# Performance work log

Hardware: AMD Instinct MI355X
Metric: run time of the kernel (lower is better)

## Reference

```python
import jax, jax.numpy as jnp
import numpy as np

HEADS = 8
EPS = 1e-5
CONV_DIMS = [(16, 32), (32, 64), (64, 128), (128, 256), (256, 128), (128, 128)]


def _bn(x, g, b):
    # BatchNorm over the node dimension (training-mode batch statistics)
    m = x.mean(0)
    v = x.var(0)
    return (x - m) * jax.lax.rsqrt(v + EPS) * g + b


def _feast(x, src, dst, W, U, c, bias, n):
    # FeaStConv: q_h = softmax_h(u_h.(x_j - x_i) + c_h); out_i = mean_j sum_h q_h * (W_h x_j) + bias
    q = jax.nn.softmax((x[src] - x[dst]) @ U + c, axis=-1)          # [E, H]
    f = (x[src] @ W).reshape(src.shape[0], HEADS, -1)               # [E, H, C_out]
    msg = jnp.einsum('ehc,eh->ec', f, q)                            # [E, C_out]
    agg = jax.ops.segment_sum(msg, dst, num_segments=n)
    cnt = jax.ops.segment_sum(jnp.ones_like(dst, dtype=msg.dtype), dst, num_segments=n)
    return agg / cnt[:, None] + bias


def reference(pos, x, g0, b0, lin0_W, lin0_b,
              W0, U0, C0, B0, gc0, bc0,
              W1, U1, C1, B1, gc1, bc1,
              W2, U2, C2, B2, gc2, bc2,
              W3, U3, C3, B3, gc3, bc3,
              W4, U4, C4, B4, gc4, bc4,
              W5, U5, C5, B5, gc5, bc5,
              lin1_W, lin1_b, lin2_W, lin2_b, edge_index):
    n = pos.shape[0]
    loops = jnp.arange(n, dtype=edge_index.dtype)                   # PyG FeaStConv adds self-loops
    src = jnp.concatenate([edge_index[0], loops])
    dst = jnp.concatenate([edge_index[1], loops])

    h = _bn(pos, g0, b0)
    h = jnp.concatenate([h, x], axis=1)
    h = jax.nn.relu(h @ lin0_W + lin0_b)

    convs = [(W0, U0, C0, B0, gc0, bc0), (W1, U1, C1, B1, gc1, bc1),
             (W2, U2, C2, B2, gc2, bc2), (W3, U3, C3, B3, gc3, bc3),
             (W4, U4, C4, B4, gc4, bc4), (W5, U5, C5, B5, gc5, bc5)]
    for W, U, c, bias, g, b in convs:
        h = _feast(h, src, dst, W, U, c, bias, n)
        h = jax.nn.relu(_bn(h, g, b))

    h = jax.nn.relu(h @ lin1_W + lin1_b)
    return h @ lin2_W + lin2_b


def setup_inputs() -> dict:
    key = jax.random.key(0)
    N, E = 10000, 160000
    ks = iter(jax.random.split(key, 64))
    d = {}
    d['pos'] = jax.random.normal(next(ks), (N, 2), jnp.float32)
    d['x'] = jax.random.normal(next(ks), (N, 2), jnp.float32)
    d['edge_index'] = jax.random.randint(next(ks), (2, E), 0, N, dtype=jnp.int32)

    def lin(k, i, o):
        return jax.random.normal(k, (i, o), jnp.float32) * np.float32(1.0 / np.sqrt(i))

    d['g0'] = jnp.ones(2, jnp.float32); d['b0'] = jnp.zeros(2, jnp.float32)
    d['lin0_W'] = lin(next(ks), 4, 16); d['lin0_b'] = jnp.zeros(16, jnp.float32)
    for i, (ci, co) in enumerate(CONV_DIMS):
        d[f'W{i}'] = lin(next(ks), ci, HEADS * co)
        d[f'U{i}'] = lin(next(ks), ci, HEADS)
        d[f'C{i}'] = jnp.zeros(HEADS, jnp.float32)
        d[f'B{i}'] = jnp.zeros(co, jnp.float32)
        d[f'gc{i}'] = jnp.ones(co, jnp.float32)
        d[f'bc{i}'] = jnp.zeros(co, jnp.float32)
    d['lin1_W'] = lin(next(ks), 128, 64); d['lin1_b'] = jnp.zeros(64, jnp.float32)
    d['lin2_W'] = lin(next(ks), 64, 2); d['lin2_b'] = jnp.zeros(2, jnp.float32)
    return d
```

## Files before the change

kernel.cpp:

```cpp
#include <hip/hip_runtime.h>
#include <hip/hip_bf16.h>
#include <math.h>

#define HEADS 8
#define EPS 1e-5f

typedef __attribute__((ext_vector_type(8))) _Float16 half8;
typedef __attribute__((ext_vector_type(4))) _Float16 half4;
typedef __attribute__((ext_vector_type(2))) _Float16 half2v;
typedef __attribute__((ext_vector_type(4))) float f32x4;

__device__ __forceinline__ unsigned short f2h(float f) {
    union { _Float16 h; unsigned short u; } v;
    v.h = (_Float16)f;
    return v.u;
}

__global__ void k_deg(const int* __restrict__ ei, int* __restrict__ deg, int E, int N) {
    int e = blockIdx.x * blockDim.x + threadIdx.x;
    int E2 = E + N;
    if (e >= E2) return;
    int dst = (e < E) ? ei[E + e] : (e - E);
    atomicAdd(&deg[dst], 1);
}

__global__ void k_scan(const int* __restrict__ deg, int* __restrict__ row_ptr, int n) {
    __shared__ int part[1024];
    int t = threadIdx.x;
    int chunk = (n + 1023) >> 10;
    int begin = t * chunk;
    int end = begin + chunk;
    if (begin > n) begin = n;
    if (end > n) end = n;
    int s = 0;
    for (int i = begin; i < end; ++i) s += deg[i];
    part[t] = s;
    __syncthreads();
    for (int off = 1; off < 1024; off <<= 1) {
        int v = (t >= off) ? part[t - off] : 0;
        __syncthreads();
        part[t] += v;
        __syncthreads();
    }
    int run = (t == 0) ? 0 : part[t - 1];
    for (int i = begin; i < end; ++i) { row_ptr[i] = run; run += deg[i]; }
    if (t == 1023) row_ptr[n] = part[1023];
}

__global__ void k_fill(const int* __restrict__ ei, const int* __restrict__ row_ptr,
                       int* __restrict__ fill, int* __restrict__ src_sorted, int E, int N) {
    int e = blockIdx.x * blockDim.x + threadIdx.x;
    int E2 = E + N;
    if (e >= E2) return;
    int srcv, dst;
    if (e < E) { srcv = ei[e]; dst = ei[E + e]; } else { srcv = e - E; dst = srcv; }
    int p = atomicAdd(&fill[dst], 1);
    src_sorted[row_ptr[dst] + p] = srcv;
}

__global__ void k_pack(const float* __restrict__ W0, const float* __restrict__ W1,
                       const float* __restrict__ W2, const float* __restrict__ W3,
                       const float* __restrict__ W4, const float* __restrict__ W5,
                       unsigned short* __restrict__ Bp) {
    int idx = blockIdx.x * blockDim.x + threadIdx.x;
    const int CI[6]  = {16, 32, 64, 128, 256, 128};
    const int CO[6]  = {32, 64, 128, 256, 128, 128};
    const int COP[6] = {64, 64, 128, 256, 128, 128};
    const int OFF[7] = {0, 8192, 24576, 90112, 352256, 614400, 745472};
    if (idx >= OFF[6]) return;
    int L = 0;
    while (idx >= OFF[L + 1]) ++L;
    const float* W = L == 0 ? W0 : L == 1 ? W1 : L == 2 ? W2 : L == 3 ? W3 : L == 4 ? W4 : W5;
    int rel = idx - OFF[L];
    int j = rel & 7;
    int lane = (rel >> 3) & 63;
    int t = rel >> 9;
    int nT = COP[L] >> 4;
    int nt = t % nT, kt = t / nT;
    int kk = kt * 32 + ((lane >> 4) << 3) + j;
    int c  = (nt << 4) + (lane & 15);
    int ci = CI[L], co = CO[L];
    float v = 0.f;
    if (c < co) {
        int h = kk / ci, ko = kk % ci;
        v = W[ko * (HEADS * co) + h * co + c];
    }
    Bp[idx] = f2h(v);
}

__global__ void k_pos_stats(const float* __restrict__ pos, float* __restrict__ stats, int n) {
    int gid = blockIdx.x * blockDim.x + threadIdx.x;
    int stride = gridDim.x * blockDim.x;
    float s0 = 0, s1 = 0, q0 = 0, q1 = 0;
    for (int i = gid; i < n; i += stride) {
        float a = pos[i * 2], b = pos[i * 2 + 1];
        s0 += a; s1 += b; q0 += a * a; q1 += b * b;
    }
    __shared__ float red[256][4];
    int t = threadIdx.x;
    red[t][0] = s0; red[t][1] = s1; red[t][2] = q0; red[t][3] = q1;
    __syncthreads();
    for (int off = 128; off > 0; off >>= 1) {
        if (t < off) {
            red[t][0] += red[t + off][0]; red[t][1] += red[t + off][1];
            red[t][2] += red[t + off][2]; red[t][3] += red[t + off][3];
        }
        __syncthreads();
    }
    if (t == 0) {
        atomicAdd(&stats[0], red[0][0]); atomicAdd(&stats[1], red[0][1]);
        atomicAdd(&stats[2], red[0][2]); atomicAdd(&stats[3], red[0][3]);
    }
}

__global__ void k_front(const float* __restrict__ pos, const float* __restrict__ x,
                        const float* __restrict__ stats, const float* __restrict__ g0,
                        const float* __restrict__ b0, const float* __restrict__ W,
                        const float* __restrict__ bias, const float* __restrict__ U0,
                        _Float16* __restrict__ out, float* __restrict__ xu0, int n) {
    int i = blockIdx.x * blockDim.x + threadIdx.x;
    if (i >= n) return;
    float invn = 1.0f / (float)n;
    float in4[4];
    #pragma unroll
    for (int j = 0; j < 2; ++j) {
        float m = stats[j] * invn;
        float v = stats[2 + j] * invn - m * m;
        in4[j] = (pos[i * 2 + j] - m) * rsqrtf(v + EPS) * g0[j] + b0[j];
    }
    in4[2] = x[i * 2]; in4[3] = x[i * 2 + 1];
    float o16[16];
    #pragma unroll
    for (int o = 0; o < 16; ++o) {
        float s = bias[o];
        #pragma unroll
        for (int j = 0; j < 4; ++j) s += in4[j] * W[j * 16 + o];
        o16[o] = fmaxf(s, 0.f);
        out[i * 16 + o] = (_Float16)o16[o];
    }
    #pragma unroll
    for (int hh = 0; hh < 8; ++hh) {
        float p = 0.f;
        #pragma unroll
        for (int k = 0; k < 16; ++k) p += o16[k] * U0[k * 8 + hh];
        xu0[i * 8 + hh] = p;
    }
}

__device__ __forceinline__ void chunk_softmax(const float* __restrict__ xu,
        const int* __restrict__ srcs, int base, int cnt, int lane,
        float4 xi0, float4 xi1, float4 c0, float4 c1, float dinv,
        float* __restrict__ qrow , int* __restrict__ srow ) {
    if (lane < cnt) {
        int s = srcs[base + lane];
        float4 xs0 = *(const float4*)(xu + (size_t)s * 8);
        float4 xs1 = *(const float4*)(xu + (size_t)s * 8 + 4);
        float t[8];
        t[0] = xs0.x - xi0.x + c0.x; t[1] = xs0.y - xi0.y + c0.y;
        t[2] = xs0.z - xi0.z + c0.z; t[3] = xs0.w - xi0.w + c0.w;
        t[4] = xs1.x - xi1.x + c1.x; t[5] = xs1.y - xi1.y + c1.y;
        t[6] = xs1.z - xi1.z + c1.z; t[7] = xs1.w - xi1.w + c1.w;
        float mx = t[0];
        #pragma unroll
        for (int h = 1; h < 8; ++h) mx = fmaxf(mx, t[h]);
        float sum = 0.f;
        #pragma unroll
        for (int h = 0; h < 8; ++h) { t[h] = __expf(t[h] - mx); sum += t[h]; }
        float qs = dinv / sum;
        float4 q0 = {t[0] * qs, t[1] * qs, t[2] * qs, t[3] * qs};
        float4 q1 = {t[4] * qs, t[5] * qs, t[6] * qs, t[7] * qs};
        *(float4*)(qrow + lane * 8) = q0;
        *(float4*)(qrow + lane * 8 + 4) = q1;
        srow[lane] = s;
    }
}

template<int V>
__global__ __launch_bounds__(256) void k_gather_big(const _Float16* __restrict__ hin,
        const float* __restrict__ xu, const float* __restrict__ chead,
        const int* __restrict__ row_ptr, const int* __restrict__ srcs,
        unsigned short* __restrict__ S, int n, int ci) {
    __shared__ float qbuf[4][64 * 8];
    __shared__ int   sbuf[4][64];
    int w = threadIdx.x >> 6, lane = threadIdx.x & 63;
    int i = blockIdx.x * 4 + w;
    if (i >= n) return;
    int rp0 = row_ptr[i], rp1 = row_ptr[i + 1];
    float dinv = 1.f / (float)(rp1 - rp0);
    float4 xi0 = *(const float4*)(xu + (size_t)i * 8);
    float4 xi1 = *(const float4*)(xu + (size_t)i * 8 + 4);
    float4 c0 = *(const float4*)chead;
    float4 c1 = *(const float4*)(chead + 4);
    int kb = lane * V;
    float acc[8][V];
    #pragma unroll
    for (int hh = 0; hh < 8; ++hh)
        #pragma unroll
        for (int v = 0; v < V; ++v) acc[hh][v] = 0.f;

    for (int base = rp0; base < rp1; base += 64) {
        int cnt = rp1 - base; if (cnt > 64) cnt = 64;
        chunk_softmax(xu, srcs, base, cnt, lane, xi0, xi1, c0, c1, dinv, qbuf[w], sbuf[w]);
        for (int j = 0; j < cnt; ++j) {
            int s = sbuf[w][j];
            const float4* qr = (const float4*)(qbuf[w] + j * 8);
            float4 q0 = qr[0], q1 = qr[1];
            float q[8] = {q0.x, q0.y, q0.z, q0.w, q1.x, q1.y, q1.z, q1.w};
            const _Float16* hs = hin + (size_t)s * ci + kb;
            float xv[V];
            if (V == 4) { half4 f = *(const half4*)hs; xv[0] = (float)f[0]; xv[1] = (float)f[1]; xv[2] = (float)f[2]; xv[3] = (float)f[3]; }
            else if (V == 2) { half2v f = *(const half2v*)hs; xv[0] = (float)f[0]; xv[1] = (float)f[1]; }
            else xv[0] = (float)hs[0];
            #pragma unroll
            for (int hh = 0; hh < 8; ++hh)
                #pragma unroll
                for (int v = 0; v < V; ++v) acc[hh][v] += q[hh] * xv[v];
        }
    }
    #pragma unroll
    for (int hh = 0; hh < 8; ++hh) {
        unsigned short o[V];
        #pragma unroll
        for (int v = 0; v < V; ++v) o[v] = f2h(acc[hh][v]);
        unsigned short* sp = S + (size_t)i * 8 * ci + hh * ci + kb;
        if (V == 4)      *(ushort4*)sp = *(ushort4*)o;
        else if (V == 2) *(ushort2*)sp = *(ushort2*)o;
        else             sp[0] = o[0];
    }
}

template<int V2>
__global__ __launch_bounds__(256) void k_gather_small(const _Float16* __restrict__ hin,
        const float* __restrict__ xu, const float* __restrict__ chead,
        const int* __restrict__ row_ptr, const int* __restrict__ srcs,
        unsigned short* __restrict__ S, int n) {
    const int ci = 8 * V2;
    __shared__ float qbuf[4][64 * 8];
    __shared__ int   sbuf[4][64];
    int w = threadIdx.x >> 6, lane = threadIdx.x & 63;
    int i = blockIdx.x * 4 + w;
    if (i >= n) return;
    int rp0 = row_ptr[i], rp1 = row_ptr[i + 1];
    float dinv = 1.f / (float)(rp1 - rp0);
    float4 xi0 = *(const float4*)(xu + (size_t)i * 8);
    float4 xi1 = *(const float4*)(xu + (size_t)i * 8 + 4);
    float4 c0 = *(const float4*)chead;
    float4 c1 = *(const float4*)(chead + 4);
    int hh = lane >> 3;
    int kb = (lane & 7) * V2;
    float acc[V2];
    #pragma unroll
    for (int v = 0; v < V2; ++v) acc[v] = 0.f;

    for (int base = rp0; base < rp1; base += 64) {
        int cnt = rp1 - base; if (cnt > 64) cnt = 64;
        chunk_softmax(xu, srcs, base, cnt, lane, xi0, xi1, c0, c1, dinv, qbuf[w], sbuf[w]);
        for (int j = 0; j < cnt; ++j) {
            int s = sbuf[w][j];
            float qh = qbuf[w][j * 8 + hh];
            const _Float16* hs = hin + (size_t)s * ci + kb;
            float xv[V2];
            if (V2 == 4) { half4 f = *(const half4*)hs; xv[0] = (float)f[0]; xv[1] = (float)f[1]; xv[2] = (float)f[2]; xv[3] = (float)f[3]; }
            else { half2v f = *(const half2v*)hs; xv[0] = (float)f[0]; xv[1] = (float)f[1]; }
            #pragma unroll
            for (int v = 0; v < V2; ++v) acc[v] += qh * xv[v];
        }
    }
    unsigned short o[V2];
    #pragma unroll
    for (int v = 0; v < V2; ++v) o[v] = f2h(acc[v]);
    unsigned short* sp = S + (size_t)i * 8 * ci + hh * ci + kb;
    if (V2 == 4) *(ushort4*)sp = *(ushort4*)o;
    else         *(ushort2*)sp = *(ushort2*)o;
}

__global__ __launch_bounds__(256) void k_gemm_stats(const unsigned short* __restrict__ A,
        const unsigned short* __restrict__ Bp, float* __restrict__ z,
        float* __restrict__ stats, int M, int K, int co, int nTtot) {
    int tid = threadIdx.x;
    int w = tid >> 6, lane = tid & 63;
    int quad = lane >> 4, l16 = lane & 15;
    int m0 = blockIdx.x * 64;
    int n0 = blockIdx.y * 64;
    int nt0 = n0 >> 4;
    int m = m0 + w * 16 + l16;
    int mc = m < M ? m : M - 1;
    const half8* Ap = (const half8*)(A + (size_t)mc * K) + quad;
    const half8* Bb = (const half8*)Bp;
    f32x4 acc[4] = {};
    int nsteps = K >> 5;
    for (int ks = 0; ks < nsteps; ++ks) {
        half8 a = Ap[ks * 4];
        long bbase = ((long)ks * nTtot + nt0) * 64 + lane;
        #pragma unroll
        for (int ct = 0; ct < 4; ++ct) {
            half8 b = Bb[bbase + ct * 64];
            acc[ct] = __builtin_amdgcn_mfma_f32_16x16x32_f16(a, b, acc[ct], 0, 0, 0);
        }
    }
    __shared__ float sred[64][4];
    __shared__ float qred[64][4];
    #pragma unroll
    for (int ct = 0; ct < 4; ++ct) {
        int colb = ct * 16 + l16;
        int col = n0 + colb;
        float s = 0.f, q = 0.f;
        #pragma unroll
        for (int r = 0; r < 4; ++r) {
            int row = m0 + w * 16 + quad * 4 + r;
            bool ok = row < M;
            float v = ok ? acc[ct][r] : 0.f;
            if (ok && col < co) z[(size_t)row * co + col] = v;
            s += v; q += v * v;
        }
        s += __shfl_xor(s, 16, 64); q += __shfl_xor(q, 16, 64);
        s += __shfl_xor(s, 32, 64); q += __shfl_xor(q, 32, 64);
        if (quad == 0) { sred[colb][w] = s; qred[colb][w] = q; }
    }
    __syncthreads();
    if (tid < 64 && (n0 + tid) < co) {
        float s = sred[tid][0] + sred[tid][1] + sred[tid][2] + sred[tid][3];
        float q = qred[tid][0] + qred[tid][1] + qred[tid][2] + qred[tid][3];
        atomicAdd(&stats[n0 + tid], s);
        atomicAdd(&stats[co + n0 + tid], q);
    }
}

template<int V>
__global__ __launch_bounds__(256) void k_bnx(const float* __restrict__ z,
        const float* __restrict__ stats, const float* __restrict__ g,
        const float* __restrict__ b, const float* __restrict__ Un,
        _Float16* __restrict__ hout, float* __restrict__ xun, int n, int co) {
    int w = threadIdx.x >> 6, lane = threadIdx.x & 63;
    int node = blockIdx.x * 4 + w;
    if (node >= n) return;
    int c0 = lane * V;
    bool act = c0 < co;
    float invn = 1.f / (float)n;
    float hv[V];
    #pragma unroll
    for (int v = 0; v < V; ++v) hv[v] = 0.f;
    if (act) {
        const float* zp = z + (size_t)node * co + c0;
        float zv[V];
        if (V == 4) { float4 f = *(const float4*)zp; zv[0] = f.x; zv[1] = f.y; zv[2] = f.z; zv[3] = f.w; }
        else if (V == 2) { float2 f = *(const float2*)zp; zv[0] = f.x; zv[1] = f.y; }
        else zv[0] = zp[0];
        #pragma unroll
        for (int v = 0; v < V; ++v) {
            int cch = c0 + v;
            float mm = stats[cch] * invn;
            float vr = stats[co + cch] * invn - mm * mm;
            hv[v] = fmaxf((zv[v] - mm) * rsqrtf(vr + EPS) * g[cch] + b[cch], 0.f);
        }
        _Float16* hp = hout + (size_t)node * co + c0;
        if (V == 4) { half4 f = {(_Float16)hv[0], (_Float16)hv[1], (_Float16)hv[2], (_Float16)hv[3]}; *(half4*)hp = f; }
        else if (V == 2) { half2v f = {(_Float16)hv[0], (_Float16)hv[1]}; *(half2v*)hp = f; }
        else hp[0] = (_Float16)hv[0];
    }
    if (Un) {
        float p[8];
        #pragma unroll
        for (int hh = 0; hh < 8; ++hh) p[hh] = 0.f;
        if (act) {
            #pragma unroll
            for (int v = 0; v < V; ++v)
                #pragma unroll
                for (int hh = 0; hh < 8; ++hh) p[hh] += hv[v] * Un[(c0 + v) * 8 + hh];
        }
        #pragma unroll
        for (int hh = 0; hh < 8; ++hh) {
            #pragma unroll
            for (int off = 32; off; off >>= 1) p[hh] += __shfl_xor(p[hh], off, 64);
        }
        float mine = 0.f;
        #pragma unroll
        for (int hh = 0; hh < 8; ++hh) if (lane == hh) mine = p[hh];
        if (lane < 8) xun[node * 8 + lane] = mine;
    }
}

__global__ __launch_bounds__(256) void k_bnlin(const float* __restrict__ z,
        const float* __restrict__ stats, const float* __restrict__ g,
        const float* __restrict__ b, const float* __restrict__ W1,
        const float* __restrict__ b1, const float* __restrict__ W2,
        const float* __restrict__ b2, float* __restrict__ out, int n) {
    __shared__ float hbuf[4][128];
    int w = threadIdx.x >> 6, lane = threadIdx.x & 63;
    int node = blockIdx.x * 4 + w;
    if (node >= n) return;
    float invn = 1.f / (float)n;
    float2 zv = *(const float2*)(z + (size_t)node * 128 + lane * 2);
    float zr[2] = {zv.x, zv.y};
    #pragma unroll
    for (int v = 0; v < 2; ++v) {
        int c = lane * 2 + v;
        float mm = stats[c] * invn;
        float vr = stats[128 + c] * invn - mm * mm;
        hbuf[w][c] = fmaxf((zr[v] - mm) * rsqrtf(vr + EPS) * g[c] + b[c], 0.f);
    }
    float s = b1[lane];
    #pragma unroll 8
    for (int k = 0; k < 128; ++k) s += hbuf[w][k] * W1[k * 64 + lane];
    float r = fmaxf(s, 0.f);
    float p0 = r * W2[lane * 2];
    float p1 = r * W2[lane * 2 + 1];
    #pragma unroll
    for (int off = 32; off > 0; off >>= 1) {
        p0 += __shfl_down(p0, off, 64);
        p1 += __shfl_down(p1, off, 64);
    }
    if (lane == 0) {
        out[node * 2] = p0 + b2[0];
        out[node * 2 + 1] = p1 + b2[1];
    }
}

extern "C" void kernel_launch(void* const* d_in, const int* in_sizes, int n_in,
                              void* d_out, int out_size, void* d_ws, size_t ws_size,
                              hipStream_t stream) {
    const float* pos    = (const float*)d_in[0];
    const float* x      = (const float*)d_in[1];
    const int*   ei     = (const int*)d_in[2];
    const float* g0     = (const float*)d_in[3];
    const float* b0     = (const float*)d_in[4];
    const float* lin0_W = (const float*)d_in[5];
    const float* lin0_b = (const float*)d_in[6];
    const float* lin1_W = (const float*)d_in[43];
    const float* lin1_b = (const float*)d_in[44];
    const float* lin2_W = (const float*)d_in[45];
    const float* lin2_b = (const float*)d_in[46];

    int N = in_sizes[0] / 2;
    int E = in_sizes[2] / 2;
    int E2 = E + N;

    static const int CI[6]  = {16, 32, 64, 128, 256, 128};
    static const int CO[6]  = {32, 64, 128, 256, 128, 128};
    static const int COP[6] = {64, 64, 128, 256, 128, 128};
    static const int BPOFF[6] = {0, 8192, 24576, 90112, 352256, 614400};

    char* p = (char*)d_ws;
    auto alloc = [&](size_t bytes) -> char* {
        char* r = p;
        p += (bytes + 255) & ~(size_t)255;
        return r;
    };
    unsigned short* BpAll = (unsigned short*)alloc(745472ull * 2);
    char* zr = alloc(((size_t)2 * N + 4 + 6 * 512) * 4);
    int*   deg      = (int*)zr;
    int*   fill     = deg + N;
    float* pstats   = (float*)(fill + N);
    float* statsAll = pstats + 4;
    size_t zr_bytes = ((size_t)2 * N + 4 + 6 * 512) * 4;

    int* row_ptr    = (int*)alloc(((size_t)N + 1) * 4);
    int* src_sorted = (int*)alloc((size_t)E2 * 4);
    float* xu       = (float*)alloc((size_t)N * 8 * 4);
    unsigned short* S = (unsigned short*)alloc((size_t)N * 2048 * 2);
    float* z        = (float*)alloc((size_t)N * 256 * 4);
    _Float16* hA    = (_Float16*)alloc((size_t)N * 256 * 2);
    _Float16* hB    = (_Float16*)alloc((size_t)N * 256 * 2);

    hipMemsetAsync(zr, 0, zr_bytes, stream);

    const int tpb = 256;
    k_deg<<<(E2 + tpb - 1) / tpb, tpb, 0, stream>>>(ei, deg, E, N);
    k_scan<<<1, 1024, 0, stream>>>(deg, row_ptr, N);
    k_fill<<<(E2 + tpb - 1) / tpb, tpb, 0, stream>>>(ei, row_ptr, fill, src_sorted, E, N);
    k_pack<<<(745472 + tpb - 1) / tpb, tpb, 0, stream>>>(
        (const float*)d_in[7], (const float*)d_in[13], (const float*)d_in[19],
        (const float*)d_in[25], (const float*)d_in[31], (const float*)d_in[37], BpAll);
    k_pos_stats<<<64, 256, 0, stream>>>(pos, pstats, N);
    k_front<<<(N + tpb - 1) / tpb, tpb, 0, stream>>>(pos, x, pstats, g0, b0, lin0_W, lin0_b,
                                                     (const float*)d_in[8], hA, xu, N);

    _Float16* hin = hA;
    _Float16* hout = hB;
    for (int L = 0; L < 6; ++L) {
        int ci = CI[L], co = CO[L], coP = COP[L];
        const float* Ch = (const float*)d_in[7 + L * 6 + 2];
        const float* gc = (const float*)d_in[7 + L * 6 + 4];
        const float* bc = (const float*)d_in[7 + L * 6 + 5];
        const float* Un = (L < 5) ? (const float*)d_in[7 + (L + 1) * 6 + 1] : nullptr;
        int K = HEADS * ci;
        float* statsL = statsAll + L * 512;

        int ggrid = (N + 3) / 4;
        if (ci == 16)       k_gather_small<2><<<ggrid, 256, 0, stream>>>(hin, xu, Ch, row_ptr, src_sorted, S, N);
        else if (ci == 32)  k_gather_small<4><<<ggrid, 256, 0, stream>>>(hin, xu, Ch, row_ptr, src_sorted, S, N);
        else if (ci == 64)  k_gather_big<1><<<ggrid, 256, 0, stream>>>(hin, xu, Ch, row_ptr, src_sorted, S, N, ci);
        else if (ci == 128) k_gather_big<2><<<ggrid, 256, 0, stream>>>(hin, xu, Ch, row_ptr, src_sorted, S, N, ci);
        else                k_gather_big<4><<<ggrid, 256, 0, stream>>>(hin, xu, Ch, row_ptr, src_sorted, S, N, ci);

        dim3 g((N + 63) / 64, coP / 64);
        k_gemm_stats<<<g, 256, 0, stream>>>(S, BpAll + BPOFF[L], z, statsL, N, K, co, coP / 16);

        int bgrid = (N + 3) / 4;
        if (L < 5) {
            if (co >= 256)      k_bnx<4><<<bgrid, 256, 0, stream>>>(z, statsL, gc, bc, Un, hout, xu, N, co);
            else if (co >= 128) k_bnx<2><<<bgrid, 256, 0, stream>>>(z, statsL, gc, bc, Un, hout, xu, N, co);
            else                k_bnx<1><<<bgrid, 256, 0, stream>>>(z, statsL, gc, bc, Un, hout, xu, N, co);
            _Float16* t = hin; hin = hout; hout = t;
        } else {
            k_bnlin<<<bgrid, 256, 0, stream>>>(z, statsL, gc, bc, lin1_W, lin1_b, lin2_W, lin2_b,
                                               (float*)d_out, N);
        }
    }
}
```

Measured before the change: 444.6 us.

## Merge setup kernels into two launches and unroll gather edge loop by two

The weight-pack, degree-count and position-statistics kernels are combined into one launch that dispatches on block index, and the CSR fill and front MLP are combined into a second launch. This cuts the number of small setup kernel launches from six to three and lets independent setup work run concurrently. The per-edge accumulation loops in both gather kernels now process two neighbours per iteration so more feature loads are in flight at once. The cost is higher register pressure in the gather kernels and more branching inside the merged setup kernels.

```diff
diff --git a/kernel.cpp b/kernel.cpp
--- a/kernel.cpp
+++ b/kernel.cpp
@@ -16,12 +16,71 @@
     return v.u;
 }
 
-__global__ void k_deg(const int* __restrict__ ei, int* __restrict__ deg, int E, int N) {
-    int e = blockIdx.x * blockDim.x + threadIdx.x;
-    int E2 = E + N;
-    if (e >= E2) return;
-    int dst = (e < E) ? ei[E + e] : (e - E);
-    atomicAdd(&deg[dst], 1);
+#define PACK_TOTAL 745472
+#define PACK_BLOCKS 2912
+
+__global__ void k_setup1(const float* __restrict__ W0, const float* __restrict__ W1,
+                         const float* __restrict__ W2, const float* __restrict__ W3,
+                         const float* __restrict__ W4, const float* __restrict__ W5,
+                         unsigned short* __restrict__ Bp,
+                         const int* __restrict__ ei, int* __restrict__ deg,
+                         const float* __restrict__ pos, float* __restrict__ pstats,
+                         int E, int N, int degBlocks) {
+    int b = blockIdx.x, tid = threadIdx.x;
+    if (b < PACK_BLOCKS) {
+        int idx = b * 256 + tid;
+        const int CI[6]  = {16, 32, 64, 128, 256, 128};
+        const int CO[6]  = {32, 64, 128, 256, 128, 128};
+        const int COP[6] = {64, 64, 128, 256, 128, 128};
+        const int OFF[7] = {0, 8192, 24576, 90112, 352256, 614400, 745472};
+        int L = 0;
+        while (idx >= OFF[L + 1]) ++L;
+        const float* W = L == 0 ? W0 : L == 1 ? W1 : L == 2 ? W2 : L == 3 ? W3 : L == 4 ? W4 : W5;
+        int rel = idx - OFF[L];
+        int j = rel & 7;
+        int lane = (rel >> 3) & 63;
+        int t = rel >> 9;
+        int nT = COP[L] >> 4;
+        int nt = t % nT, kt = t / nT;
+        int kk = kt * 32 + ((lane >> 4) << 3) + j;
+        int c  = (nt << 4) + (lane & 15);
+        int ci = CI[L], co = CO[L];
+        float v = 0.f;
+        if (c < co) {
+            int h = kk / ci, ko = kk % ci;
+            v = W[ko * (HEADS * co) + h * co + c];
+        }
+        Bp[idx] = f2h(v);
+    } else if (b < PACK_BLOCKS + degBlocks) {
+        int e = (b - PACK_BLOCKS) * 256 + tid;
+        int E2 = E + N;
+        if (e < E2) {
+            int dst = (e < E) ? ei[E + e] : (e - E);
+            atomicAdd(&deg[dst], 1);
+        }
+    } else {
+        int gid = (b - PACK_BLOCKS - degBlocks) * 256 + tid;
+        int stride = 64 * 256;
+        float s0 = 0, s1 = 0, q0 = 0, q1 = 0;
+        for (int i = gid; i < N; i += stride) {
+            float a = pos[i * 2], bb = pos[i * 2 + 1];
+            s0 += a; s1 += bb; q0 += a * a; q1 += bb * bb;
+        }
+        __shared__ float red[256][4];
+        red[tid][0] = s0; red[tid][1] = s1; red[tid][2] = q0; red[tid][3] = q1;
+        __syncthreads();
+        for (int off = 128; off > 0; off >>= 1) {
+            if (tid < off) {
+                red[tid][0] += red[tid + off][0]; red[tid][1] += red[tid + off][1];
+                red[tid][2] += red[tid + off][2]; red[tid][3] += red[tid + off][3];
+            }
+            __syncthreads();
+        }
+        if (tid == 0) {
+            atomicAdd(&pstats[0], red[0][0]); atomicAdd(&pstats[1], red[0][1]);
+            atomicAdd(&pstats[2], red[0][2]); atomicAdd(&pstats[3], red[0][3]);
+        }
+    }
 }
 
 __global__ void k_scan(const int* __restrict__ deg, int* __restrict__ row_ptr, int n) {
@@ -47,110 +106,59 @@
     if (t == 1023) row_ptr[n] = part[1023];
 }
 
-__global__ void k_fill(const int* __restrict__ ei, const int* __restrict__ row_ptr,
-                       int* __restrict__ fill, int* __restrict__ src_sorted, int E, int N) {
-    int e = blockIdx.x * blockDim.x + threadIdx.x;
-    int E2 = E + N;
-    if (e >= E2) return;
-    int srcv, dst;
-    if (e < E) { srcv = ei[e]; dst = ei[E + e]; } else { srcv = e - E; dst = srcv; }
-    int p = atomicAdd(&fill[dst], 1);
-    src_sorted[row_ptr[dst] + p] = srcv;
-}
-
-__global__ void k_pack(const float* __restrict__ W0, const float* __restrict__ W1,
-                       const float* __restrict__ W2, const float* __restrict__ W3,
-                       const float* __restrict__ W4, const float* __restrict__ W5,
-                       unsigned short* __restrict__ Bp) {
-    int idx = blockIdx.x * blockDim.x + threadIdx.x;
-    const int CI[6]  = {16, 32, 64, 128, 256, 128};
-    const int CO[6]  = {32, 64, 128, 256, 128, 128};
-    const int COP[6] = {64, 64, 128, 256, 128, 128};
-    const int OFF[7] = {0, 8192, 24576, 90112, 352256, 614400, 745472};
-    if (idx >= OFF[6]) return;
-    int L = 0;
-    while (idx >= OFF[L + 1]) ++L;
-    const float* W = L == 0 ? W0 : L == 1 ? W1 : L == 2 ? W2 : L == 3 ? W3 : L == 4 ? W4 : W5;
-    int rel = idx - OFF[L];
-    int j = rel & 7;
-    int lane = (rel >> 3) & 63;
-    int t = rel >> 9;
-    int nT = COP[L] >> 4;
-    int nt = t % nT, kt = t / nT;
-    int kk = kt * 32 + ((lane >> 4) << 3) + j;
-    int c  = (nt << 4) + (lane & 15);
-    int ci = CI[L], co = CO[L];
-    float v = 0.f;
-    if (c < co) {
-        int h = kk / ci, ko = kk % ci;
-        v = W[ko * (HEADS * co) + h * co + c];
-    }
-    Bp[idx] = f2h(v);
-}
-
-__global__ void k_pos_stats(const float* __restrict__ pos, float* __restrict__ stats, int n) {
-    int gid = blockIdx.x * blockDim.x + threadIdx.x;
-    int stride = gridDim.x * blockDim.x;
-    float s0 = 0, s1 = 0, q0 = 0, q1 = 0;
-    for (int i = gid; i < n; i += stride) {
-        float a = pos[i * 2], b = pos[i * 2 + 1];
-        s0 += a; s1 += b; q0 += a * a; q1 += b * b;
-    }
-    __shared__ float red[256][4];
-    int t = threadIdx.x;
-    red[t][0] = s0; red[t][1] = s1; red[t][2] = q0; red[t][3] = q1;
-    __syncthreads();
-    for (int off = 128; off > 0; off >>= 1) {
-        if (t < off) {
-            red[t][0] += red[t + off][0]; red[t][1] += red[t + off][1];
-            red[t][2] += red[t + off][2]; red[t][3] += red[t + off][3];
-        }
-        __syncthreads();
-    }
-    if (t == 0) {
-        atomicAdd(&stats[0], red[0][0]); atomicAdd(&stats[1], red[0][1]);
-        atomicAdd(&stats[2], red[0][2]); atomicAdd(&stats[3], red[0][3]);
-    }
-}
-
-__global__ void k_front(const float* __restrict__ pos, const float* __restrict__ x,
-                        const float* __restrict__ stats, const float* __restrict__ g0,
-                        const float* __restrict__ b0, const float* __restrict__ W,
-                        const float* __restrict__ bias, const float* __restrict__ U0,
-                        _Float16* __restrict__ out, float* __restrict__ xu0, int n) {
-    int i = blockIdx.x * blockDim.x + threadIdx.x;
-    if (i >= n) return;
-    float invn = 1.0f / (float)n;
-    float in4[4];
-    #pragma unroll
-    for (int j = 0; j < 2; ++j) {
-        float m = stats[j] * invn;
-        float v = stats[2 + j] * invn - m * m;
-        in4[j] = (pos[i * 2 + j] - m) * rsqrtf(v + EPS) * g0[j] + b0[j];
-    }
-    in4[2] = x[i * 2]; in4[3] = x[i * 2 + 1];
-    float o16[16];
-    #pragma unroll
-    for (int o = 0; o < 16; ++o) {
-        float s = bias[o];
-        #pragma unroll
-        for (int j = 0; j < 4; ++j) s += in4[j] * W[j * 16 + o];
-        o16[o] = fmaxf(s, 0.f);
-        out[i * 16 + o] = (_Float16)o16[o];
-    }
-    #pragma unroll
-    for (int hh = 0; hh < 8; ++hh) {
-        float p = 0.f;
-        #pragma unroll
-        for (int k = 0; k < 16; ++k) p += o16[k] * U0[k * 8 + hh];
-        xu0[i * 8 + hh] = p;
+__global__ void k_setup2(const int* __restrict__ ei, const int* __restrict__ row_ptr,
+                         int* __restrict__ fill, int* __restrict__ src_sorted,
+                         const float* __restrict__ pos, const float* __restrict__ x,
+                         const float* __restrict__ pstats, const float* __restrict__ g0,
+                         const float* __restrict__ b0, const float* __restrict__ W,
+                         const float* __restrict__ bias, const float* __restrict__ U0,
+                         _Float16* __restrict__ out, float* __restrict__ xu0,
+                         int E, int N, int fillBlocks) {
+    int b = blockIdx.x, tid = threadIdx.x;
+    if (b < fillBlocks) {
+        int e = b * 256 + tid;
+        int E2 = E + N;
+        if (e < E2) {
+            int srcv, dst;
+            if (e < E) { srcv = ei[e]; dst = ei[E + e]; } else { srcv = e - E; dst = srcv; }
+            int p = atomicAdd(&fill[dst], 1);
+            src_sorted[row_ptr[dst] + p] = srcv;
+        }
+    } else {
+        int i = (b - fillBlocks) * 256 + tid;
+        if (i >= N) return;
+        float invn = 1.0f / (float)N;
+        float in4[4];
+        #pragma unroll
+        for (int j = 0; j < 2; ++j) {
+            float m = pstats[j] * invn;
+            float v = pstats[2 + j] * invn - m * m;
+            in4[j] = (pos[i * 2 + j] - m) * rsqrtf(v + EPS) * g0[j] + b0[j];
+        }
+        in4[2] = x[i * 2]; in4[3] = x[i * 2 + 1];
+        float o16[16];
+        #pragma unroll
+        for (int o = 0; o < 16; ++o) {
+            float s = bias[o];
+            #pragma unroll
+            for (int j = 0; j < 4; ++j) s += in4[j] * W[j * 16 + o];
+            o16[o] = fmaxf(s, 0.f);
+            out[i * 16 + o] = (_Float16)o16[o];
+        }
+        #pragma unroll
+        for (int hh = 0; hh < 8; ++hh) {
+            float p = 0.f;
+            #pragma unroll
+            for (int k = 0; k < 16; ++k) p += o16[k] * U0[k * 8 + hh];
+            xu0[i * 8 + hh] = p;
+        }
     }
 }
 
 __device__ __forceinline__ void chunk_softmax(const float* __restrict__ xu,
         const int* __restrict__ srcs, int base, int cnt, int lane,
         float4 xi0, float4 xi1, float4 c0, float4 c1, float dinv,
-        float* __restrict__ qrow , int* __restrict__ srow ) {
+        float* __restrict__ qrow, int* __restrict__ srow) {
     if (lane < cnt) {
         int s = srcs[base + lane];
         float4 xs0 = *(const float4*)(xu + (size_t)s * 8);
@@ -201,20 +209,52 @@
     for (int base = rp0; base < rp1; base += 64) {
         int cnt = rp1 - base; if (cnt > 64) cnt = 64;
         chunk_softmax(xu, srcs, base, cnt, lane, xi0, xi1, c0, c1, dinv, qbuf[w], sbuf[w]);
-        for (int j = 0; j < cnt; ++j) {
-            int s = sbuf[w][j];
-            const float4* qr = (const float4*)(qbuf[w] + j * 8);
-            float4 q0 = qr[0], q1 = qr[1];
-            float q[8] = {q0.x, q0.y, q0.z, q0.w, q1.x, q1.y, q1.z, q1.w};
-            const _Float16* hs = hin + (size_t)s * ci + kb;
-            float xv[V];
-            if (V == 4) { half4 f = *(const half4*)hs; xv[0] = (float)f[0]; xv[1] = (float)f[1]; xv[2] = (float)f[2]; xv[3] = (float)f[3]; }
-            else if (V == 2) { half2v f = *(const half2v*)hs; xv[0] = (float)f[0]; xv[1] = (float)f[1]; }
-            else xv[0] = (float)hs[0];
+        int j = 0;
+        for (; j + 1 < cnt; j += 2) {
+            int s0 = sbuf[w][j], s1 = sbuf[w][j + 1];
+            const _Float16* h0 = hin + (size_t)s0 * ci + kb;
+            const _Float16* h1 = hin + (size_t)s1 * ci + kb;
+            float xv0[V], xv1[V];
+            if (V == 4) {
+                half4 f0 = *(const half4*)h0, f1 = *(const half4*)h1;
+                #pragma unroll
+                for (int v = 0; v < 4; ++v) { xv0[v] = (float)f0[v]; xv1[v] = (float)f1[v]; }
+            } else if (V == 2) {
+                half2v f0 = *(const half2v*)h0, f1 = *(const half2v*)h1;
+                #pragma unroll
+                for (int v = 0; v < 2; ++v) { xv0[v] = (float)f0[v]; xv1[v] = (float)f1[v]; }
+            } else { xv0[0] = (float)h0[0]; xv1[0] = (float)h1[0]; }
+            const float4* qa = (const float4*)(qbuf[w] + j * 8);
+            const float4* qc = (const float4*)(qbuf[w] + (j + 1) * 8);
+            float4 qa0 = qa[0], qa1 = qa[1], qb0 = qc[0], qb1 = qc[1];
+            float qA[8] = {qa0.x, qa0.y, qa0.z, qa0.w, qa1.x, qa1.y, qa1.z, qa1.w};
+            float qB[8] = {qb0.x, qb0.y, qb0.z, qb0.w, qb1.x, qb1.y, qb1.z, qb1.w};
             #pragma unroll
             for (int hh = 0; hh < 8; ++hh)
                 #pragma unroll
-                for (int v = 0; v < V; ++v) acc[hh][v] += q[hh] * xv[v];
+                for (int v = 0; v < V; ++v)
+                    acc[hh][v] += qA[hh] * xv0[v] + qB[hh] * xv1[v];
+        }
+        if (j < cnt) {
+            int s0 = sbuf[w][j];
+            const _Float16* h0 = hin + (size_t)s0 * ci + kb;
+            float xv0[V];
+            if (V == 4) {
+                half4 f = *(const half4*)h0;
+                for (int v = 0; v < 4; ++v) xv0[v] = (float)f[v];
+            } else if (V == 2) {
+                half2v f = *(const half2v*)h0;
+                for (int v = 0; v < 2; ++v) xv0[v] = (float)f[v];
+            } else {
+                xv0[0] = (float)h0[0];
+            }
+            const float4* qa = (const float4*)(qbuf[w] + j * 8);
+            float4 qa0 = qa[0], qa1 = qa[1];
+            float qA[8] = {qa0.x, qa0.y, qa0.z, qa0.w, qa1.x, qa1.y, qa1.z, qa1.w};
+            #pragma unroll
+            for (int hh = 0; hh < 8; ++hh)
+                #pragma unroll
+                for (int v = 0; v < V; ++v) acc[hh][v] += qA[hh] * xv0[v];
         }
     }
     #pragma unroll
@@ -255,15 +295,40 @@
     for (int base = rp0; base < rp1; base += 64) {
         int cnt = rp1 - base; if (cnt > 64) cnt = 64;
         chunk_softmax(xu, srcs, base, cnt, lane, xi0, xi1, c0, c1, dinv, qbuf[w], sbuf[w]);
-        for (int j = 0; j < cnt; ++j) {
-            int s = sbuf[w][j];
-            float qh = qbuf[w][j * 8 + hh];
-            const _Float16* hs = hin + (size_t)s * ci + kb;
-            float xv[V2];
-            if (V2 == 4) { half4 f = *(const half4*)hs; xv[0] = (float)f[0]; xv[1] = (float)f[1]; xv[2] = (float)f[2]; xv[3] = (float)f[3]; }
-            else { half2v f = *(const half2v*)hs; xv[0] = (float)f[0]; xv[1] = (float)f[1]; }
-            #pragma unroll
-            for (int v = 0; v < V2; ++v) acc[v] += qh * xv[v];
+        int j = 0;
+        for (; j + 1 < cnt; j += 2) {
+            int s0 = sbuf[w][j], s1 = sbuf[w][j + 1];
+            const _Float16* h0 = hin + (size_t)s0 * ci + kb;
+            const _Float16* h1 = hin + (size_t)s1 * ci + kb;
+            float xv0[V2], xv1[V2];
+            if (V2 == 4) {
+                half4 f0 = *(const half4*)h0, f1 = *(const half4*)h1;
+                #pragma unroll
+                for (int v = 0; v < 4; ++v) { xv0[v] = (float)f0[v]; xv1[v] = (float)f1[v]; }
+            } else {
+                half2v f0 = *(const half2v*)h0, f1 = *(const half2v*)h1;
+                #pragma unroll
+                for (int v = 0; v < 2; ++v) { xv0[v] = (float)f0[v]; xv1[v] = (float)f1[v]; }
+            }
+            float q0 = qbuf[w][j * 8 + hh];
+            float q1 = qbuf[w][(j + 1) * 8 + hh];
+            #pragma unroll
+            for (int v = 0; v < V2; ++v) acc[v] += q0 * xv0[v] + q1 * xv1[v];
+        }
+        if (j < cnt) {
+            int s0 = sbuf[w][j];
+            const _Float16* h0 = hin + (size_t)s0 * ci + kb;
+            float xv0[V2];
+            if (V2 == 4) {
+                half4 f = *(const half4*)h0;
+                for (int v = 0; v < 4; ++v) xv0[v] = (float)f[v];
+            } else {
+                half2v f = *(const half2v*)h0;
+                for (int v = 0; v < 2; ++v) xv0[v] = (float)f[v];
+            }
+            float q0 = qbuf[w][j * 8 + hh];
+            #pragma unroll
+            for (int v = 0; v < V2; ++v) acc[v] += q0 * xv0[v];
         }
     }
     unsigned short o[V2];
@@ -446,7 +511,7 @@
         p += (bytes + 255) & ~(size_t)255;
         return r;
     };
-    unsigned short* BpAll = (unsigned short*)alloc(745472ull * 2);
+    unsigned short* BpAll = (unsigned short*)alloc((size_t)PACK_TOTAL * 2);
     char* zr = alloc(((size_t)2 * N + 4 + 6 * 512) * 4);
     int*   deg      = (int*)zr;
     int*   fill     = deg + N;
@@ -465,15 +530,18 @@
     hipMemsetAsync(zr, 0, zr_bytes, stream);
 
     const int tpb = 256;
-    k_deg<<<(E2 + tpb - 1) / tpb, tpb, 0, stream>>>(ei, deg, E, N);
+    int degBlocks = (E2 + tpb - 1) / tpb;
+    int fillBlocks = degBlocks;
+    int frontBlocks = (N + tpb - 1) / tpb;
+
+    k_setup1<<<PACK_BLOCKS + degBlocks + 64, tpb, 0, stream>>>(
+        (const float*)d_in[7], (const float*)d_in[13], (const float*)d_in[19],
+        (const float*)d_in[25], (const float*)d_in[31], (const float*)d_in[37], BpAll,
+        ei, deg, pos, pstats, E, N, degBlocks);
     k_scan<<<1, 1024, 0, stream>>>(deg, row_ptr, N);
-    k_fill<<<(E2 + tpb - 1) / tpb, tpb, 0, stream>>>(ei, row_ptr, fill, src_sorted, E, N);
-    k_pack<<<(745472 + tpb - 1) / tpb, tpb, 0, stream>>>(
-        (const float*)d_in[7], (const float*)d_in[13], (const float*)d_in[19],
-        (const float*)d_in[25], (const float*)d_in[31], (const float*)d_in[37], BpAll);
-    k_pos_stats<<<64, 256, 0, stream>>>(pos, pstats, N);
-    k_front<<<(N + tpb - 1) / tpb, tpb, 0, stream>>>(pos, x, pstats, g0, b0, lin0_W, lin0_b,
-                                                     (const float*)d_in[8], hA, xu, N);
+    k_setup2<<<fillBlocks + frontBlocks, tpb, 0, stream>>>(
+        ei, row_ptr, fill, src_sorted, pos, x, pstats, g0, b0, lin0_W, lin0_b,
+        (const float*)d_in[8], hA, xu, E, N, fillBlocks);
 
     _Float16* hin = hA;
     _Float16* hout = hB;
```

Result: no change. 449.3 us (+1.1%).
